# Kernel optimization log

Hardware: AMD Instinct MI355X
Metric: run time of the kernel (lower is better)

Reference implementation:

```python
import jax, jax.numpy as jnp
import numpy as np

B, N, HS = 2, 2048, 1024
H, D = 16, 64
GRID = 16           # crop_size // patch_size
SEG = 20            # d_dim = h_dim = w_dim = 2*(64//3//2)


def setup_inputs() -> dict:
    key = jax.random.key(0)
    ks = jax.random.split(key, 5)
    s = 0.02
    return {
        "hidden_states": jax.random.normal(ks[0], (B, N, HS), jnp.float32),
        "Wq": jax.random.normal(ks[1], (HS, HS), jnp.float32) * s,
        "bq": jnp.zeros((HS,), jnp.float32),
        "Wk": jax.random.normal(ks[2], (HS, HS), jnp.float32) * s,
        "bk": jnp.zeros((HS,), jnp.float32),
        "Wv": jax.random.normal(ks[3], (HS, HS), jnp.float32) * s,
        "bv": jnp.zeros((HS,), jnp.float32),
        "Wp": jax.random.normal(ks[4], (HS, HS), jnp.float32) * s,
        "bp": jnp.zeros((HS,), jnp.float32),
    }


def _rope(x, pos):
    # x: [B, H, N, d], pos: [N] int. Faithful to rotate_queries_or_keys:
    # sin/cos are TILED (concat of two copies), rotation is pairwise interleaved.
    d = x.shape[-1]
    omega = 1.0 / (10000.0 ** (jnp.arange(d // 2, dtype=x.dtype) / (d / 2.0)))
    freq = pos.astype(x.dtype)[:, None] * omega          # [N, d/2]
    sin = jnp.tile(jnp.sin(freq), (1, 2))                # [N, d]
    cos = jnp.tile(jnp.cos(freq), (1, 2))
    xp = x.reshape(x.shape[:-1] + (d // 2, 2))
    rot = jnp.stack([-xp[..., 1], xp[..., 0]], axis=-1).reshape(x.shape)
    return x * cos + rot * sin


def _apply_rope3d(qk, fpos, hpos, wpos):
    parts, s = [], 0
    for pos in (fpos, hpos, wpos):
        parts.append(_rope(qk[..., s:s + SEG], pos))
        s += SEG
    parts.append(qk[..., s:])  # pass-through remainder (4 dims)
    return jnp.concatenate(parts, axis=-1)


def reference(hidden_states, Wq, bq, Wk, bk, Wv, bv, Wp, bp):
    b, n, _ = hidden_states.shape

    def heads(x):  # [B,N,HS] -> [B,H,N,D]
        return x.reshape(b, n, H, D).transpose(0, 2, 1, 3)

    q = heads(hidden_states @ Wq.T + bq)
    k = heads(hidden_states @ Wk.T + bk)
    v = heads(hidden_states @ Wv.T + bv)

    ids = jnp.arange(n)
    tpf = GRID * GRID
    fpos = ids // tpf
    rem = ids - fpos * tpf
    hpos = rem // GRID
    wpos = rem - hpos * GRID

    q = _apply_rope3d(q, fpos, hpos, wpos)
    k = _apply_rope3d(k, fpos, hpos, wpos)

    scores = jnp.einsum('bhqd,bhkd->bhqk', q, k) * (D ** -0.5)
    probs = jax.nn.softmax(scores.astype(jnp.float32), axis=-1).astype(q.dtype)
    ctx = jnp.einsum('bhqk,bhkd->bqhd', probs, v).reshape(b, n, HS)
    return ctx @ Wp.T + bp
```

## Files before the change

kernel.cpp:

```cpp
#include <hip/hip_runtime.h>
#include <hip/hip_bf16.h>
#include <math.h>

#define BB    2
#define NN    2048
#define HSZ   1024
#define NH    16
#define HD    64
#define SEGW  20

#define LOG2E  1.4426950408889634f
#define QSCALE (0.125f * LOG2E)
#define DTHR   8.0f

typedef unsigned short u16;
typedef unsigned int   u32;
using bf16x8 = __attribute__((ext_vector_type(8))) short;
using f32x4  = __attribute__((ext_vector_type(4))) float;
using f32x16 = __attribute__((ext_vector_type(16))) float;

__device__ __forceinline__ u16 f2b(float f) {
    union { float f; u32 u; } x; x.f = f;
    u32 r = x.u + 0x7FFF + ((x.u >> 16) & 1);
    return (u16)(r >> 16);
}
__device__ __forceinline__ u16 f2bc(float f) {
    __hip_bfloat16 h = __float2bfloat16(f);
    return *reinterpret_cast<u16*>(&h);
}

__device__ __forceinline__ void gload16(void* lds, const void* g) {
    __builtin_amdgcn_global_load_lds(
        (const __attribute__((address_space(1))) void*)g,
        (__attribute__((address_space(3))) void*)lds, 16, 0, 0);
}

__device__ __forceinline__ void pswap(u32& a, u32& b) {
    asm volatile("v_permlane32_swap_b32 %0, %1" : "+v"(a), "+v"(b));
}

__global__ __launch_bounds__(256)
void cast_k(const float* __restrict__ hs, const float* __restrict__ Wq,
            const float* __restrict__ Wk, const float* __restrict__ Wv,
            const float* __restrict__ Wp, u16* __restrict__ hsb,
            u16* __restrict__ wqb, u16* __restrict__ wkb,
            u16* __restrict__ wvb, u16* __restrict__ wpb) {
    size_t idx = ((size_t)blockIdx.x * 256 + threadIdx.x) * 4;
    const float* s; u16* d; size_t o;
    const size_t HSN = 4194304, WN = 1048576;
    if      (idx < HSN)          { s = hs; d = hsb; o = idx; }
    else if (idx < HSN + WN)     { s = Wq; d = wqb; o = idx - HSN; }
    else if (idx < HSN + 2*WN)   { s = Wk; d = wkb; o = idx - HSN - WN; }
    else if (idx < HSN + 3*WN)   { s = Wv; d = wvb; o = idx - HSN - 2*WN; }
    else                         { s = Wp; d = wpb; o = idx - HSN - 3*WN; }
    float4 v = *(const float4*)(s + o);
    u32 lo = f2b(v.x) | ((u32)f2b(v.y) << 16);
    u32 hi = f2b(v.z) | ((u32)f2b(v.w) << 16);
    *(uint2*)(d + o) = uint2{lo, hi};
}

__global__ void rope_table_k(float* __restrict__ tab) {
    int n = blockIdx.x, d = threadIdx.x;
    float c = 1.f, s = 0.f;
    if (d < 3 * SEGW) {
        int seg = d / SEGW;
        int jj  = (d % SEGW) % (SEGW / 2);
        int rem = n & 255;
        int pos = (seg == 0) ? (n >> 8) : ((seg == 1) ? (rem >> 4) : (rem & 15));
        float omega = powf(10000.f, -(float)jj / 10.f);
        float fr = (float)pos * omega;
        s = sinf(fr); c = cosf(fr);
    }
    tab[(n * 64 + d) * 2 + 0] = c;
    tab[(n * 64 + d) * 2 + 1] = s;
}

__device__ __forceinline__
void gemm_body(const u16* __restrict__ X, const u16* __restrict__ Wb,
               const float* __restrict__ bias, void* __restrict__ out,
               const float* __restrict__ tab, int mode) {
    __shared__ u16 As[2][128 * 32];
    __shared__ u16 Bs[2][128 * 32];

    const int t  = threadIdx.x;
    const int w  = t >> 6;
    const int l  = t & 63;
    const int flat = blockIdx.x + (blockIdx.y << 3);
    const int o0 = (flat >> 5) * 128;
    const int m0 = (flat & 31) * 128;
    const int wr = (w >> 1) * 64;
    const int wc = (w & 1) * 64;

    const int ch  = (w << 6) + l;
    const int rA0 = ch >> 2,         cA0 = (((ch & 3) ^ (rA0 & 3))) * 8;
    const int rA1 = (ch + 256) >> 2, cA1 = (((ch & 3) ^ (rA1 & 3))) * 8;
    const int kbyte = (((l >> 4) ^ (l & 3)) << 4);

    f32x4 acc[4][4] = {};

    gload16(As[0] + ((w << 6)) * 8,       X  + (size_t)(m0 + rA0) * HSZ + cA0);
    gload16(As[0] + (256 + (w << 6)) * 8, X  + (size_t)(m0 + rA1) * HSZ + cA1);
    gload16(Bs[0] + ((w << 6)) * 8,       Wb + (size_t)(o0 + rA0) * HSZ + cA0);
    gload16(Bs[0] + (256 + (w << 6)) * 8, Wb + (size_t)(o0 + rA1) * HSZ + cA1);
    __syncthreads();

    int cur = 0;
    for (int k0 = 0; k0 < HSZ; k0 += 32, cur ^= 1) {
        if (k0 + 32 < HSZ) {
            int kn = k0 + 32;
            gload16(As[cur ^ 1] + ((w << 6)) * 8,       X  + (size_t)(m0 + rA0) * HSZ + kn + cA0);
            gload16(As[cur ^ 1] + (256 + (w << 6)) * 8, X  + (size_t)(m0 + rA1) * HSZ + kn + cA1);
            gload16(Bs[cur ^ 1] + ((w << 6)) * 8,       Wb + (size_t)(o0 + rA0) * HSZ + kn + cA0);
            gload16(Bs[cur ^ 1] + (256 + (w << 6)) * 8, Wb + (size_t)(o0 + rA1) * HSZ + kn + cA1);
        }
        bf16x8 af[4], bfr[4];
#pragma unroll
        for (int i = 0; i < 4; ++i) {
            int row = wr + i * 16 + (l & 15);
            af[i] = *(const bf16x8*)((const char*)As[cur] + row * 64 + kbyte);
        }
#pragma unroll
        for (int j = 0; j < 4; ++j) {
            int row = wc + j * 16 + (l & 15);
            bfr[j] = *(const bf16x8*)((const char*)Bs[cur] + row * 64 + kbyte);
        }
        __builtin_amdgcn_s_setprio(1);
#pragma unroll
        for (int i = 0; i < 4; ++i)
#pragma unroll
            for (int j = 0; j < 4; ++j)
                acc[i][j] = __builtin_amdgcn_mfma_f32_16x16x32_bf16(af[i], bfr[j], acc[i][j], 0, 0, 0);
        __builtin_amdgcn_s_setprio(0);
        __syncthreads();
    }

#pragma unroll
    for (int j = 0; j < 4; ++j) {
        int oc = o0 + wc + j * 16 + (l & 15);
        int h  = oc >> 6;
        int d  = oc & 63;
        float bv = bias[oc];
        if (mode == 2) {
#pragma unroll
            for (int rt = 0; rt < 4; ++rt) {
                int base = m0 + wr + rt * 16 + (l >> 4) * 4;
                int b_ = base >> 11, n0 = base & (NN - 1);
                u16 e[4];
#pragma unroll
                for (int r = 0; r < 4; ++r) e[r] = f2b(acc[rt][j][r] + bv);
                u32 lo = e[0] | ((u32)e[1] << 16);
                u32 hi = e[2] | ((u32)e[3] << 16);
                u16* vp = (u16*)out + (((size_t)b_ * NH + h) * HD + d) * NN + n0;
                *(uint2*)vp = uint2{lo, hi};
            }
        } else if (mode == 3) {
#pragma unroll
            for (int rt = 0; rt < 4; ++rt)
#pragma unroll
                for (int r = 0; r < 4; ++r) {
                    int m = m0 + wr + rt * 16 + (l >> 4) * 4 + r;
                    ((float*)out)[(size_t)m * HSZ + oc] = acc[rt][j][r] + bv;
                }
        } else {
            float scl = (mode == 0) ? QSCALE : 1.f;
#pragma unroll
            for (int rt = 0; rt < 4; ++rt)
#pragma unroll
                for (int r = 0; r < 4; ++r) {
                    int m = m0 + wr + rt * 16 + (l >> 4) * 4 + r;
                    int n = m & (NN - 1), b_ = m >> 11;
                    float v = acc[rt][j][r] + bv;
                    float2 cs = ((const float2*)tab)[n * 64 + d];
                    float part = __shfl_xor(v, 1);
                    float vr = (l & 1) ? fmaf(part, cs.y, v * cs.x)
                                       : fmaf(-part, cs.y, v * cs.x);
                    u16* qp = (u16*)out + (((size_t)b_ * NH + h) * NN + n) * HD + d;
                    *qp = f2b(vr * scl);
                }
        }
    }
}

__global__ __launch_bounds__(256)
void qkv_k(const u16* __restrict__ X,
           const u16* __restrict__ Wq, const u16* __restrict__ Wk, const u16* __restrict__ Wv,
           const float* __restrict__ bq, const float* __restrict__ bk, const float* __restrict__ bv,
           u16* __restrict__ qo, u16* __restrict__ ko, u16* __restrict__ vo,
           const float* __restrict__ tab) {
    int z = blockIdx.z;
    const u16* W   = (z == 0) ? Wq : (z == 1) ? Wk : Wv;
    const float* b = (z == 0) ? bq : (z == 1) ? bk : bv;
    u16* o         = (z == 0) ? qo : (z == 1) ? ko : vo;
    gemm_body(X, W, b, o, tab, z);
}

__global__ __launch_bounds__(256)
void projo_k(const u16* __restrict__ X, const u16* __restrict__ W,
             const float* __restrict__ b, float* __restrict__ out) {
    gemm_body(X, W, b, out, nullptr, 3);
}

__global__ __launch_bounds__(256)
void attn_mfma_k(const u16* __restrict__ Qb, const u16* __restrict__ Kb,
                 const u16* __restrict__ Vtb, u16* __restrict__ ctxb) {
    __shared__ u16 KVs[2][2][64 * 64];

    const int t = threadIdx.x, w = t >> 6, l = t & 63;
    const int h = l >> 5;
    int f  = blockIdx.y * 16 + blockIdx.x;
    int bh = (f & 7) * 4 + ((f >> 3) & 3);
    int qt = f >> 5;
    const int b_ = bh >> 4, hd = bh & 15;

    const u16* Qg = Qb + ((size_t)bh * NN + qt * 128) * HD;
    const u16* Kg = Kb + (size_t)bh * NN * HD;
    const u16* Vg = Vtb + (size_t)bh * HD * NN;

    const int xr   = (l & 7) << 4;
    const int h16  = h * 16;
    const int rowo = (l & 31) * 128;
    int kb4[4];
#pragma unroll
    for (int ks = 0; ks < 4; ++ks) kb4[ks] = ((ks * 32) | h16) ^ xr;

    const int ch  = w * 64 + l;
    const int r0  = ch >> 3,          sl0 = (ch & 7) ^ (r0 & 7);
    const int r1  = (ch + 256) >> 3,  sl1 = (ch & 7) ^ (r1 & 7);

#pragma unroll
    for (int s = 0; s < 4; ++s) {
        int c = s * 256 + ch;
        int row = c >> 3, sl = (c & 7) ^ (row & 7);
        gload16(&KVs[0][0][0] + (s * 256 + w * 64) * 8, Qg + row * HD + sl * 8);
    }
    __syncthreads();
    bf16x8 qf[4];
    {
        const char* Ql = (const char*)&KVs[0][0][0];
        int qrow = (w * 32 + (l & 31)) * 128;
#pragma unroll
        for (int ks = 0; ks < 4; ++ks)
            qf[ks] = *(const bf16x8*)(Ql + qrow + kb4[ks]);
    }
    __syncthreads();

    gload16(&KVs[0][0][0] + (w * 64) * 8,        Kg + (size_t)r0 * HD + sl0 * 8);
    gload16(&KVs[0][0][0] + (256 + w * 64) * 8,  Kg + (size_t)r1 * HD + sl1 * 8);
    gload16(&KVs[0][1][0] + (w * 64) * 8,        Vg + (size_t)r0 * NN + sl0 * 8);
    gload16(&KVs[0][1][0] + (256 + w * 64) * 8,  Vg + (size_t)r1 * NN + sl1 * 8);
    __syncthreads();

    float m_i = -INFINITY, l_i = 0.f;
    f32x16 oa0 = {}, oa1 = {};

    int cur = 0;
    for (int kt = 0; kt < NN / 64; ++kt, cur ^= 1) {
        if (kt + 1 < NN / 64) {
            int nx = (kt + 1) * 64;
            gload16(&KVs[cur ^ 1][0][0] + (w * 64) * 8,       Kg + (size_t)(nx + r0) * HD + sl0 * 8);
            gload16(&KVs[cur ^ 1][0][0] + (256 + w * 64) * 8, Kg + (size_t)(nx + r1) * HD + sl1 * 8);
            gload16(&KVs[cur ^ 1][1][0] + (w * 64) * 8,       Vg + (size_t)r0 * NN + nx + sl0 * 8);
            gload16(&KVs[cur ^ 1][1][0] + (256 + w * 64) * 8, Vg + (size_t)r1 * NN + nx + sl1 * 8);
        }

        const char* Kl = (const char*)&KVs[cur][0][0];
        f32x16 sa0 = {}, sa1 = {};
        __builtin_amdgcn_s_setprio(1);
#pragma unroll
        for (int ks = 0; ks < 4; ++ks) {
            bf16x8 k0 = *(const bf16x8*)(Kl + rowo + kb4[ks]);
            bf16x8 k1 = *(const bf16x8*)(Kl + 4096 + rowo + kb4[ks]);
            sa0 = __builtin_amdgcn_mfma_f32_32x32x16_bf16(k0, qf[ks], sa0, 0, 0, 0);
            sa1 = __builtin_amdgcn_mfma_f32_32x32x16_bf16(k1, qf[ks], sa1, 0, 0, 0);
        }
        __builtin_amdgcn_s_setprio(0);

        float mx8[8];
#pragma unroll
        for (int j = 0; j < 8; ++j)
            mx8[j] = fmaxf(fmaxf(sa0[j], sa0[j + 8]), fmaxf(sa1[j], sa1[j + 8]));
        float pm = fmaxf(fmaxf(fmaxf(mx8[0], mx8[1]), fmaxf(mx8[2], mx8[3])),
                         fmaxf(fmaxf(mx8[4], mx8[5]), fmaxf(mx8[6], mx8[7])));
        if (__any(pm > m_i + DTHR)) {
            float mx = fmaxf(pm, __shfl_xor(pm, 32));
            float mn = fmaxf(m_i, mx);
            float alpha = __builtin_amdgcn_exp2f(m_i - mn);
            m_i = mn;
            l_i *= alpha;
#pragma unroll
            for (int r = 0; r < 16; ++r) { oa0[r] *= alpha; oa1[r] *= alpha; }
        }

        u32 o_[16];
        float ls0 = 0.f, ls1 = 0.f, ls2 = 0.f, ls3 = 0.f;
#pragma unroll
        for (int j = 0; j < 8; ++j) {
            float pa = __builtin_amdgcn_exp2f(sa0[2 * j]     - m_i);
            float pb = __builtin_amdgcn_exp2f(sa0[2 * j + 1] - m_i);
            float pc = __builtin_amdgcn_exp2f(sa1[2 * j]     - m_i);
            float pd = __builtin_amdgcn_exp2f(sa1[2 * j + 1] - m_i);
            ls0 += pa; ls1 += pb; ls2 += pc; ls3 += pd;
            o_[j]     = (u32)f2bc(pa) | ((u32)f2bc(pb) << 16);
            o_[8 + j] = (u32)f2bc(pc) | ((u32)f2bc(pd) << 16);
        }
        l_i += (ls0 + ls1) + (ls2 + ls3);

        pswap(o_[0], o_[2]);   pswap(o_[1], o_[3]);
        pswap(o_[4], o_[6]);   pswap(o_[5], o_[7]);
        pswap(o_[8], o_[10]);  pswap(o_[9], o_[11]);
        pswap(o_[12], o_[14]); pswap(o_[13], o_[15]);

        const char* Vl = (const char*)&KVs[cur][1][0];
        __builtin_amdgcn_s_setprio(1);
#pragma unroll
        for (int ks2 = 0; ks2 < 4; ++ks2) {
            union { u32 u[4]; bf16x8 v; } fr;
            fr.u[0] = o_[4 * ks2 + 0]; fr.u[1] = o_[4 * ks2 + 1];
            fr.u[2] = o_[4 * ks2 + 2]; fr.u[3] = o_[4 * ks2 + 3];
            bf16x8 v0 = *(const bf16x8*)(Vl + rowo + kb4[ks2]);
            bf16x8 v1 = *(const bf16x8*)(Vl + 4096 + rowo + kb4[ks2]);
            oa0 = __builtin_amdgcn_mfma_f32_32x32x16_bf16(v0, fr.v, oa0, 0, 0, 0);
            oa1 = __builtin_amdgcn_mfma_f32_32x32x16_bf16(v1, fr.v, oa1, 0, 0, 0);
        }
        __builtin_amdgcn_s_setprio(0);

        __syncthreads();
    }

    float lt = l_i + __shfl_xor(l_i, 32);
    float inv = 1.f / lt;
    int n = qt * 128 + w * 32 + (l & 31);
    u16* op = ctxb + ((size_t)b_ * NN + n) * HSZ + hd * 64;
#pragma unroll
    for (int dt = 0; dt < 2; ++dt) {
        const f32x16& oa = dt ? oa1 : oa0;
#pragma unroll
        for (int rg = 0; rg < 4; ++rg) {
            int d0 = 4 * h + 8 * rg + 32 * dt;
            u16 e0 = f2bc(oa[4 * rg + 0] * inv);
            u16 e1 = f2bc(oa[4 * rg + 1] * inv);
            u16 e2 = f2bc(oa[4 * rg + 2] * inv);
            u16 e3 = f2bc(oa[4 * rg + 3] * inv);
            *(uint2*)(op + d0) = uint2{e0 | ((u32)e1 << 16), e2 | ((u32)e3 << 16)};
        }
    }
}

extern "C" void kernel_launch(void* const* d_in, const int* in_sizes, int n_in,
                              void* d_out, int out_size, void* d_ws, size_t ws_size,
                              hipStream_t stream) {
    (void)in_sizes; (void)n_in; (void)out_size; (void)ws_size;
    const float* hs = (const float*)d_in[0];
    const float* Wq = (const float*)d_in[1];
    const float* bq = (const float*)d_in[2];
    const float* Wk = (const float*)d_in[3];
    const float* bk = (const float*)d_in[4];
    const float* Wv = (const float*)d_in[5];
    const float* bv = (const float*)d_in[6];
    const float* Wp = (const float*)d_in[7];
    const float* bp = (const float*)d_in[8];

    char* ws = (char*)d_ws;
    u16*   hsb  = (u16*)(ws);
    u16*   Wqb  = (u16*)(ws + 8388608);
    u16*   Wkb  = (u16*)(ws + 10485760);
    u16*   Wvb  = (u16*)(ws + 12582912);
    u16*   Wpb  = (u16*)(ws + 14680064);
    u16*   qb   = (u16*)(ws + 16777216);
    u16*   kb   = (u16*)(ws + 25165824);
    u16*   vtb  = (u16*)(ws + 33554432);
    u16*   ctxb = (u16*)(ws + 41943040);
    float* tab  = (float*)(ws + 50331648);

    cast_k<<<8192, 256, 0, stream>>>(hs, Wq, Wk, Wv, Wp, hsb, Wqb, Wkb, Wvb, Wpb);
    rope_table_k<<<NN, 64, 0, stream>>>(tab);

    qkv_k<<<dim3(HSZ / 128, (BB * NN) / 128, 3), 256, 0, stream>>>(
        hsb, Wqb, Wkb, Wvb, bq, bk, bv, qb, kb, vtb, tab);

    attn_mfma_k<<<dim3(NN / 128, BB * NH), 256, 0, stream>>>(qb, kb, vtb, ctxb);

    projo_k<<<dim3(HSZ / 128, (BB * NN) / 128), 256, 0, stream>>>(ctxb, Wpb, bp, (float*)d_out);
}
```

Before: 140.4 us.

## Split attention KV across warp pairs and load GEMM B fragments directly from global

The attention kernel now gives each warp two 32-query subtiles and half of each 64-key tile, so one K fragment load feeds two MFMAs. Each warp pair keeps its own running max and sum, and the partial outputs are merged through shared memory at the end. The projection GEMM drops the shared-memory staging of the weight tile and loads B fragments straight from global into registers, prefetched one step ahead. This trades LDS traffic for uncoalesced global loads and more registers, plus an extra cross-warp merge with its barrier.

```diff
diff --git a/kernel.cpp b/kernel.cpp
--- a/kernel.cpp
+++ b/kernel.cpp
@@ -80,7 +80,6 @@
                const float* __restrict__ bias, void* __restrict__ out,
                const float* __restrict__ tab, int mode) {
     __shared__ u16 As[2][128 * 32];
-    __shared__ u16 Bs[2][128 * 32];
 
     const int t  = threadIdx.x;
     const int w  = t >> 6;
@@ -96,41 +95,46 @@
     const int rA1 = (ch + 256) >> 2, cA1 = (((ch & 3) ^ (rA1 & 3))) * 8;
     const int kbyte = (((l >> 4) ^ (l & 3)) << 4);
 
+    const u16* bp[4];
+#pragma unroll
+    for (int j = 0; j < 4; ++j)
+        bp[j] = Wb + (size_t)(o0 + wc + j * 16 + (l & 15)) * HSZ + ((l >> 4) << 3);
+
     f32x4 acc[4][4] = {};
-
-    gload16(As[0] + ((w << 6)) * 8,       X  + (size_t)(m0 + rA0) * HSZ + cA0);
-    gload16(As[0] + (256 + (w << 6)) * 8, X  + (size_t)(m0 + rA1) * HSZ + cA1);
-    gload16(Bs[0] + ((w << 6)) * 8,       Wb + (size_t)(o0 + rA0) * HSZ + cA0);
-    gload16(Bs[0] + (256 + (w << 6)) * 8, Wb + (size_t)(o0 + rA1) * HSZ + cA1);
+    bf16x8 bc[4], bn[4];
+
+    gload16(As[0] + ((w << 6)) * 8,       X + (size_t)(m0 + rA0) * HSZ + cA0);
+    gload16(As[0] + (256 + (w << 6)) * 8, X + (size_t)(m0 + rA1) * HSZ + cA1);
+#pragma unroll
+    for (int j = 0; j < 4; ++j) bc[j] = *(const bf16x8*)(bp[j]);
     __syncthreads();
 
     int cur = 0;
     for (int k0 = 0; k0 < HSZ; k0 += 32, cur ^= 1) {
         if (k0 + 32 < HSZ) {
             int kn = k0 + 32;
-            gload16(As[cur ^ 1] + ((w << 6)) * 8,       X  + (size_t)(m0 + rA0) * HSZ + kn + cA0);
-            gload16(As[cur ^ 1] + (256 + (w << 6)) * 8, X  + (size_t)(m0 + rA1) * HSZ + kn + cA1);
-            gload16(Bs[cur ^ 1] + ((w << 6)) * 8,       Wb + (size_t)(o0 + rA0) * HSZ + kn + cA0);
-            gload16(Bs[cur ^ 1] + (256 + (w << 6)) * 8, Wb + (size_t)(o0 + rA1) * HSZ + kn + cA1);
-        }
-        bf16x8 af[4], bfr[4];
+            gload16(As[cur ^ 1] + ((w << 6)) * 8,       X + (size_t)(m0 + rA0) * HSZ + kn + cA0);
+            gload16(As[cur ^ 1] + (256 + (w << 6)) * 8, X + (size_t)(m0 + rA1) * HSZ + kn + cA1);
+#pragma unroll
+            for (int j = 0; j < 4; ++j) bn[j] = *(const bf16x8*)(bp[j] + kn);
+        }
+        bf16x8 af[4];
 #pragma unroll
         for (int i = 0; i < 4; ++i) {
             int row = wr + i * 16 + (l & 15);
             af[i] = *(const bf16x8*)((const char*)As[cur] + row * 64 + kbyte);
         }
-#pragma unroll
-        for (int j = 0; j < 4; ++j) {
-            int row = wc + j * 16 + (l & 15);
-            bfr[j] = *(const bf16x8*)((const char*)Bs[cur] + row * 64 + kbyte);
-        }
         __builtin_amdgcn_s_setprio(1);
 #pragma unroll
         for (int i = 0; i < 4; ++i)
 #pragma unroll
             for (int j = 0; j < 4; ++j)
-                acc[i][j] = __builtin_amdgcn_mfma_f32_16x16x32_bf16(af[i], bfr[j], acc[i][j], 0, 0, 0);
+                acc[i][j] = __builtin_amdgcn_mfma_f32_16x16x32_bf16(af[i], bc[j], acc[i][j], 0, 0, 0);
         __builtin_amdgcn_s_setprio(0);
+        if (k0 + 32 < HSZ) {
+#pragma unroll
+            for (int j = 0; j < 4; ++j) bc[j] = bn[j];
+        }
         __syncthreads();
     }
 
@@ -204,9 +208,12 @@
 void attn_mfma_k(const u16* __restrict__ Qb, const u16* __restrict__ Kb,
                  const u16* __restrict__ Vtb, u16* __restrict__ ctxb) {
     __shared__ u16 KVs[2][2][64 * 64];
+    __shared__ float2 MLs[2][2][32];
 
     const int t = threadIdx.x, w = t >> 6, l = t & 63;
     const int h = l >> 5;
+    const int qh = w & 1, kh = w >> 1;
+    const int q = l & 31;
     int f  = blockIdx.y * 16 + blockIdx.x;
     int bh = (f & 7) * 4 + ((f >> 3) & 3);
     int qt = f >> 5;
@@ -216,16 +223,15 @@
     const u16* Kg = Kb + (size_t)bh * NN * HD;
     const u16* Vg = Vtb + (size_t)bh * HD * NN;
 
-    const int xr   = (l & 7) << 4;
-    const int h16  = h * 16;
-    const int rowo = (l & 31) * 128;
+    const int xr  = (l & 7) << 4;
+    const int h16 = h * 16;
     int kb4[4];
 #pragma unroll
     for (int ks = 0; ks < 4; ++ks) kb4[ks] = ((ks * 32) | h16) ^ xr;
 
     const int ch  = w * 64 + l;
-    const int r0  = ch >> 3,          sl0 = (ch & 7) ^ (r0 & 7);
-    const int r1  = (ch + 256) >> 3,  sl1 = (ch & 7) ^ (r1 & 7);
+    const int r0  = ch >> 3,         sl0 = (ch & 7) ^ (r0 & 7);
+    const int r1  = (ch + 256) >> 3, sl1 = (ch & 7) ^ (r1 & 7);
 
 #pragma unroll
     for (int s = 0; s < 4; ++s) {
@@ -234,25 +240,28 @@
         gload16(&KVs[0][0][0] + (s * 256 + w * 64) * 8, Qg + row * HD + sl * 8);
     }
     __syncthreads();
-    bf16x8 qf[4];
+    bf16x8 qf[2][4];
     {
         const char* Ql = (const char*)&KVs[0][0][0];
-        int qrow = (w * 32 + (l & 31)) * 128;
-#pragma unroll
-        for (int ks = 0; ks < 4; ++ks)
-            qf[ks] = *(const bf16x8*)(Ql + qrow + kb4[ks]);
+#pragma unroll
+        for (int qs = 0; qs < 2; ++qs)
+#pragma unroll
+            for (int ks = 0; ks < 4; ++ks)
+                qf[qs][ks] = *(const bf16x8*)(Ql + (qh * 64 + qs * 32 + q) * 128 + kb4[ks]);
     }
     __syncthreads();
 
-    gload16(&KVs[0][0][0] + (w * 64) * 8,        Kg + (size_t)r0 * HD + sl0 * 8);
-    gload16(&KVs[0][0][0] + (256 + w * 64) * 8,  Kg + (size_t)r1 * HD + sl1 * 8);
-    gload16(&KVs[0][1][0] + (w * 64) * 8,        Vg + (size_t)r0 * NN + sl0 * 8);
-    gload16(&KVs[0][1][0] + (256 + w * 64) * 8,  Vg + (size_t)r1 * NN + sl1 * 8);
+    gload16(&KVs[0][0][0] + (w * 64) * 8,       Kg + (size_t)r0 * HD + sl0 * 8);
+    gload16(&KVs[0][0][0] + (256 + w * 64) * 8, Kg + (size_t)r1 * HD + sl1 * 8);
+    gload16(&KVs[0][1][0] + (w * 64) * 8,       Vg + (size_t)r0 * NN + sl0 * 8);
+    gload16(&KVs[0][1][0] + (256 + w * 64) * 8, Vg + (size_t)r1 * NN + sl1 * 8);
     __syncthreads();
 
-    float m_i = -INFINITY, l_i = 0.f;
-    f32x16 oa0 = {}, oa1 = {};
-
+    float m_i[2] = {-INFINITY, -INFINITY};
+    float l_i[2] = {0.f, 0.f};
+    f32x16 oa[2][2] = {};
+
+    const int rowk = (kh * 32 + q) * 128;
     int cur = 0;
     for (int kt = 0; kt < NN / 64; ++kt, cur ^= 1) {
         if (kt + 1 < NN / 64) {
@@ -264,84 +273,124 @@
         }
 
         const char* Kl = (const char*)&KVs[cur][0][0];
-        f32x16 sa0 = {}, sa1 = {};
+        f32x16 sa[2] = {};
         __builtin_amdgcn_s_setprio(1);
 #pragma unroll
         for (int ks = 0; ks < 4; ++ks) {
-            bf16x8 k0 = *(const bf16x8*)(Kl + rowo + kb4[ks]);
-            bf16x8 k1 = *(const bf16x8*)(Kl + 4096 + rowo + kb4[ks]);
-            sa0 = __builtin_amdgcn_mfma_f32_32x32x16_bf16(k0, qf[ks], sa0, 0, 0, 0);
-            sa1 = __builtin_amdgcn_mfma_f32_32x32x16_bf16(k1, qf[ks], sa1, 0, 0, 0);
+            bf16x8 kf = *(const bf16x8*)(Kl + rowk + kb4[ks]);
+            sa[0] = __builtin_amdgcn_mfma_f32_32x32x16_bf16(kf, qf[0][ks], sa[0], 0, 0, 0);
+            sa[1] = __builtin_amdgcn_mfma_f32_32x32x16_bf16(kf, qf[1][ks], sa[1], 0, 0, 0);
         }
         __builtin_amdgcn_s_setprio(0);
 
-        float mx8[8];
-#pragma unroll
-        for (int j = 0; j < 8; ++j)
-            mx8[j] = fmaxf(fmaxf(sa0[j], sa0[j + 8]), fmaxf(sa1[j], sa1[j + 8]));
-        float pm = fmaxf(fmaxf(fmaxf(mx8[0], mx8[1]), fmaxf(mx8[2], mx8[3])),
-                         fmaxf(fmaxf(mx8[4], mx8[5]), fmaxf(mx8[6], mx8[7])));
-        if (__any(pm > m_i + DTHR)) {
-            float mx = fmaxf(pm, __shfl_xor(pm, 32));
-            float mn = fmaxf(m_i, mx);
-            float alpha = __builtin_amdgcn_exp2f(m_i - mn);
-            m_i = mn;
-            l_i *= alpha;
-#pragma unroll
-            for (int r = 0; r < 16; ++r) { oa0[r] *= alpha; oa1[r] *= alpha; }
-        }
-
-        u32 o_[16];
-        float ls0 = 0.f, ls1 = 0.f, ls2 = 0.f, ls3 = 0.f;
-#pragma unroll
-        for (int j = 0; j < 8; ++j) {
-            float pa = __builtin_amdgcn_exp2f(sa0[2 * j]     - m_i);
-            float pb = __builtin_amdgcn_exp2f(sa0[2 * j + 1] - m_i);
-            float pc = __builtin_amdgcn_exp2f(sa1[2 * j]     - m_i);
-            float pd = __builtin_amdgcn_exp2f(sa1[2 * j + 1] - m_i);
-            ls0 += pa; ls1 += pb; ls2 += pc; ls3 += pd;
-            o_[j]     = (u32)f2bc(pa) | ((u32)f2bc(pb) << 16);
-            o_[8 + j] = (u32)f2bc(pc) | ((u32)f2bc(pd) << 16);
-        }
-        l_i += (ls0 + ls1) + (ls2 + ls3);
-
-        pswap(o_[0], o_[2]);   pswap(o_[1], o_[3]);
-        pswap(o_[4], o_[6]);   pswap(o_[5], o_[7]);
-        pswap(o_[8], o_[10]);  pswap(o_[9], o_[11]);
-        pswap(o_[12], o_[14]); pswap(o_[13], o_[15]);
+        float pm[2];
+#pragma unroll
+        for (int qs = 0; qs < 2; ++qs) {
+            float t8[8];
+#pragma unroll
+            for (int j = 0; j < 8; ++j) t8[j] = fmaxf(sa[qs][2 * j], sa[qs][2 * j + 1]);
+            float a0 = fmaxf(t8[0], t8[1]), a1 = fmaxf(t8[2], t8[3]);
+            float a2 = fmaxf(t8[4], t8[5]), a3 = fmaxf(t8[6], t8[7]);
+            pm[qs] = fmaxf(fmaxf(a0, a1), fmaxf(a2, a3));
+        }
+        if (__any((pm[0] > m_i[0] + DTHR) | (pm[1] > m_i[1] + DTHR))) {
+#pragma unroll
+            for (int qs = 0; qs < 2; ++qs) {
+                float mx = fmaxf(pm[qs], __shfl_xor(pm[qs], 32));
+                float mn = fmaxf(m_i[qs], mx);
+                float alpha = __builtin_amdgcn_exp2f(m_i[qs] - mn);
+                m_i[qs] = mn;
+                l_i[qs] *= alpha;
+#pragma unroll
+                for (int r = 0; r < 16; ++r) { oa[qs][0][r] *= alpha; oa[qs][1][r] *= alpha; }
+            }
+        }
+
+        u32 oq[2][8];
+#pragma unroll
+        for (int qs = 0; qs < 2; ++qs) {
+            float ls = 0.f;
+#pragma unroll
+            for (int j = 0; j < 8; ++j) {
+                float pa = __builtin_amdgcn_exp2f(sa[qs][2 * j]     - m_i[qs]);
+                float pb = __builtin_amdgcn_exp2f(sa[qs][2 * j + 1] - m_i[qs]);
+                ls += pa + pb;
+                oq[qs][j] = (u32)f2bc(pa) | ((u32)f2bc(pb) << 16);
+            }
+            l_i[qs] += ls;
+            pswap(oq[qs][0], oq[qs][2]); pswap(oq[qs][1], oq[qs][3]);
+            pswap(oq[qs][4], oq[qs][6]); pswap(oq[qs][5], oq[qs][7]);
+        }
 
         const char* Vl = (const char*)&KVs[cur][1][0];
         __builtin_amdgcn_s_setprio(1);
 #pragma unroll
-        for (int ks2 = 0; ks2 < 4; ++ks2) {
-            union { u32 u[4]; bf16x8 v; } fr;
-            fr.u[0] = o_[4 * ks2 + 0]; fr.u[1] = o_[4 * ks2 + 1];
-            fr.u[2] = o_[4 * ks2 + 2]; fr.u[3] = o_[4 * ks2 + 3];
-            bf16x8 v0 = *(const bf16x8*)(Vl + rowo + kb4[ks2]);
-            bf16x8 v1 = *(const bf16x8*)(Vl + 4096 + rowo + kb4[ks2]);
-            oa0 = __builtin_amdgcn_mfma_f32_32x32x16_bf16(v0, fr.v, oa0, 0, 0, 0);
-            oa1 = __builtin_amdgcn_mfma_f32_32x32x16_bf16(v1, fr.v, oa1, 0, 0, 0);
+        for (int ks2 = 0; ks2 < 2; ++ks2) {
+            int vb = (((kh * 2 + ks2) * 32) | h16) ^ xr;
+            bf16x8 v0 = *(const bf16x8*)(Vl + q * 128 + vb);
+            bf16x8 v1 = *(const bf16x8*)(Vl + (32 + q) * 128 + vb);
+            union { u32 u[4]; bf16x8 v; } f0, f1;
+#pragma unroll
+            for (int p = 0; p < 4; ++p) {
+                f0.u[p] = oq[0][4 * ks2 + p];
+                f1.u[p] = oq[1][4 * ks2 + p];
+            }
+            oa[0][0] = __builtin_amdgcn_mfma_f32_32x32x16_bf16(v0, f0.v, oa[0][0], 0, 0, 0);
+            oa[0][1] = __builtin_amdgcn_mfma_f32_32x32x16_bf16(v1, f0.v, oa[0][1], 0, 0, 0);
+            oa[1][0] = __builtin_amdgcn_mfma_f32_32x32x16_bf16(v0, f1.v, oa[1][0], 0, 0, 0);
+            oa[1][1] = __builtin_amdgcn_mfma_f32_32x32x16_bf16(v1, f1.v, oa[1][1], 0, 0, 0);
         }
         __builtin_amdgcn_s_setprio(0);
 
         __syncthreads();
     }
 
-    float lt = l_i + __shfl_xor(l_i, 32);
-    float inv = 1.f / lt;
-    int n = qt * 128 + w * 32 + (l & 31);
-    u16* op = ctxb + ((size_t)b_ * NN + n) * HSZ + hd * 64;
-#pragma unroll
-    for (int dt = 0; dt < 2; ++dt) {
-        const f32x16& oa = dt ? oa1 : oa0;
-#pragma unroll
-        for (int rg = 0; rg < 4; ++rg) {
-            int d0 = 4 * h + 8 * rg + 32 * dt;
-            u16 e0 = f2bc(oa[4 * rg + 0] * inv);
-            u16 e1 = f2bc(oa[4 * rg + 1] * inv);
-            u16 e2 = f2bc(oa[4 * rg + 2] * inv);
-            u16 e3 = f2bc(oa[4 * rg + 3] * inv);
-            *(uint2*)(op + d0) = uint2{e0 | ((u32)e1 << 16), e2 | ((u32)e3 << 16)};
+    float lh[2];
+#pragma unroll
+    for (int qs = 0; qs < 2; ++qs) lh[qs] = l_i[qs] + __shfl_xor(l_i[qs], 32);
+
+    float* Olds = (float*)&KVs[0][0][0];
+    if (kh == 1) {
+#pragma unroll
+        for (int qs = 0; qs < 2; ++qs) {
+            int base = ((qh * 2 + qs) * 32 + q) * 256;
+#pragma unroll
+            for (int dh = 0; dh < 2; ++dh)
+#pragma unroll
+                for (int g = 0; g < 4; ++g) {
+                    int off = (128 * dh + 32 * g + 16 * h) ^ ((q & 7) << 4);
+                    float4 v4 = {oa[qs][dh][4 * g + 0], oa[qs][dh][4 * g + 1],
+                                 oa[qs][dh][4 * g + 2], oa[qs][dh][4 * g + 3]};
+                    *(float4*)((char*)Olds + base + off) = v4;
+                }
+            if (h == 0) MLs[qh][qs][q] = float2{m_i[qs], lh[qs]};
+        }
+    }
+    __syncthreads();
+    if (kh == 0) {
+#pragma unroll
+        for (int qs = 0; qs < 2; ++qs) {
+            float2 ml1 = MLs[qh][qs][q];
+            float mM = fmaxf(m_i[qs], ml1.x);
+            float w0 = __builtin_amdgcn_exp2f(m_i[qs] - mM);
+            float w1 = __builtin_amdgcn_exp2f(ml1.x - mM);
+            float inv = 1.f / (w0 * lh[qs] + w1 * ml1.y);
+            int n = qt * 128 + qh * 64 + qs * 32 + q;
+            u16* op = ctxb + ((size_t)b_ * NN + n) * HSZ + hd * 64;
+            int base = ((qh * 2 + qs) * 32 + q) * 256;
+#pragma unroll
+            for (int dh = 0; dh < 2; ++dh)
+#pragma unroll
+                for (int g = 0; g < 4; ++g) {
+                    int off = (128 * dh + 32 * g + 16 * h) ^ ((q & 7) << 4);
+                    float4 o1 = *(const float4*)((const char*)Olds + base + off);
+                    int d0 = 8 * g + 4 * h + 32 * dh;
+                    u16 e0 = f2bc((oa[qs][dh][4 * g + 0] * w0 + o1.x * w1) * inv);
+                    u16 e1 = f2bc((oa[qs][dh][4 * g + 1] * w0 + o1.y * w1) * inv);
+                    u16 e2 = f2bc((oa[qs][dh][4 * g + 2] * w0 + o1.z * w1) * inv);
+                    u16 e3 = f2bc((oa[qs][dh][4 * g + 3] * w0 + o1.w * w1) * inv);
+                    *(uint2*)(op + d0) = uint2{e0 | ((u32)e1 << 16), e2 | ((u32)e3 << 16)};
+                }
         }
     }
 }
```

After: 188.4 us. +34.2%, slower.

## Shrink QKV/output GEMM tiles to 128x64 and drop LDS swizzle

Applied to the files above, without the earlier changes.

The shared GEMM body now computes 128x64 output tiles instead of 128x128, so each of the four waves holds a 64x32 accumulator block. This doubles the grid for the QKV and output-projection launches (16x32 blocks). The change also removes the XOR swizzle on LDS loads and reads, and drops the s_setprio hints. The intent is more blocks and higher occupancy with fewer registers per block. The cost is less data reuse per block, more global traffic for the activation tiles, and likely LDS bank conflicts from the unswizzled 64-byte row stride.

```diff
diff --git a/kernel.cpp b/kernel.cpp
--- a/kernel.cpp
+++ b/kernel.cpp
@@ -80,28 +80,27 @@
                const float* __restrict__ bias, void* __restrict__ out,
                const float* __restrict__ tab, int mode) {
     __shared__ u16 As[2][128 * 32];
-    __shared__ u16 Bs[2][128 * 32];
+    __shared__ u16 Bs[2][64 * 32];
 
     const int t  = threadIdx.x;
     const int w  = t >> 6;
     const int l  = t & 63;
-    const int flat = blockIdx.x + (blockIdx.y << 3);
-    const int o0 = (flat >> 5) * 128;
+    const int flat = blockIdx.x + (blockIdx.y << 4);
+    const int o0 = (flat >> 5) * 64;
     const int m0 = (flat & 31) * 128;
     const int wr = (w >> 1) * 64;
-    const int wc = (w & 1) * 64;
-
-    const int ch  = (w << 6) + l;
-    const int rA0 = ch >> 2,         cA0 = (((ch & 3) ^ (rA0 & 3))) * 8;
-    const int rA1 = (ch + 256) >> 2, cA1 = (((ch & 3) ^ (rA1 & 3))) * 8;
-    const int kbyte = (((l >> 4) ^ (l & 3)) << 4);
-
-    f32x4 acc[4][4] = {};
+    const int wc = (w & 1) * 32;
+
+    const int chA0 = (w << 6) + l;
+    const int rA0 = chA0 >> 2,         cA0 = (chA0 & 3) * 8;
+    const int rA1 = (chA0 + 256) >> 2, cA1 = (chA0 & 3) * 8;
+    const int rB  = chA0 >> 2,         cB  = (chA0 & 3) * 8;
+
+    f32x4 acc[4][2] = {};
 
     gload16(As[0] + ((w << 6)) * 8,       X  + (size_t)(m0 + rA0) * HSZ + cA0);
     gload16(As[0] + (256 + (w << 6)) * 8, X  + (size_t)(m0 + rA1) * HSZ + cA1);
-    gload16(Bs[0] + ((w << 6)) * 8,       Wb + (size_t)(o0 + rA0) * HSZ + cA0);
-    gload16(Bs[0] + (256 + (w << 6)) * 8, Wb + (size_t)(o0 + rA1) * HSZ + cA1);
+    gload16(Bs[0] + ((w << 6)) * 8,       Wb + (size_t)(o0 + rB) * HSZ + cB);
     __syncthreads();
 
     int cur = 0;
@@ -110,34 +109,27 @@
             int kn = k0 + 32;
             gload16(As[cur ^ 1] + ((w << 6)) * 8,       X  + (size_t)(m0 + rA0) * HSZ + kn + cA0);
             gload16(As[cur ^ 1] + (256 + (w << 6)) * 8, X  + (size_t)(m0 + rA1) * HSZ + kn + cA1);
-            gload16(Bs[cur ^ 1] + ((w << 6)) * 8,       Wb + (size_t)(o0 + rA0) * HSZ + kn + cA0);
-            gload16(Bs[cur ^ 1] + (256 + (w << 6)) * 8, Wb + (size_t)(o0 + rA1) * HSZ + kn + cA1);
-        }
-        bf16x8 af[4], bfr[4];
-#pragma unroll
-        for (int i = 0; i < 4; ++i) {
-            int row = wr + i * 16 + (l & 15);
-            af[i] = *(const bf16x8*)((const char*)As[cur] + row * 64 + kbyte);
-        }
-#pragma unroll
-        for (int j = 0; j < 4; ++j) {
-            int row = wc + j * 16 + (l & 15);
-            bfr[j] = *(const bf16x8*)((const char*)Bs[cur] + row * 64 + kbyte);
-        }
-        __builtin_amdgcn_s_setprio(1);
+            gload16(Bs[cur ^ 1] + ((w << 6)) * 8,       Wb + (size_t)(o0 + rB) * HSZ + kn + cB);
+        }
+        bf16x8 af[4], bfr[2];
 #pragma unroll
         for (int i = 0; i < 4; ++i)
-#pragma unroll
-            for (int j = 0; j < 4; ++j)
+            af[i] = *(const bf16x8*)(As[cur] + (wr + i * 16 + (l & 15)) * 32 + (l >> 4) * 8);
+#pragma unroll
+        for (int j = 0; j < 2; ++j)
+            bfr[j] = *(const bf16x8*)(Bs[cur] + (wc + j * 16 + (l & 15)) * 32 + (l >> 4) * 8);
+#pragma unroll
+        for (int i = 0; i < 4; ++i)
+#pragma unroll
+            for (int j = 0; j < 2; ++j)
                 acc[i][j] = __builtin_amdgcn_mfma_f32_16x16x32_bf16(af[i], bfr[j], acc[i][j], 0, 0, 0);
-        __builtin_amdgcn_s_setprio(0);
         __syncthreads();
     }
 
-#pragma unroll
-    for (int j = 0; j < 4; ++j) {
-        int oc = o0 + wc + j * 16 + (l & 15);
-        int h  = oc >> 6;
+    const int h = o0 >> 6;
+#pragma unroll
+    for (int ct = 0; ct < 2; ++ct) {
+        int oc = o0 + wc + ct * 16 + (l & 15);
         int d  = oc & 63;
         float bv = bias[oc];
         if (mode == 2) {
@@ -147,7 +139,7 @@
                 int b_ = base >> 11, n0 = base & (NN - 1);
                 u16 e[4];
 #pragma unroll
-                for (int r = 0; r < 4; ++r) e[r] = f2b(acc[rt][j][r] + bv);
+                for (int r = 0; r < 4; ++r) e[r] = f2b(acc[rt][ct][r] + bv);
                 u32 lo = e[0] | ((u32)e[1] << 16);
                 u32 hi = e[2] | ((u32)e[3] << 16);
                 u16* vp = (u16*)out + (((size_t)b_ * NH + h) * HD + d) * NN + n0;
@@ -159,7 +151,7 @@
 #pragma unroll
                 for (int r = 0; r < 4; ++r) {
                     int m = m0 + wr + rt * 16 + (l >> 4) * 4 + r;
-                    ((float*)out)[(size_t)m * HSZ + oc] = acc[rt][j][r] + bv;
+                    ((float*)out)[(size_t)m * HSZ + oc] = acc[rt][ct][r] + bv;
                 }
         } else {
             float scl = (mode == 0) ? QSCALE : 1.f;
@@ -169,7 +161,7 @@
                 for (int r = 0; r < 4; ++r) {
                     int m = m0 + wr + rt * 16 + (l >> 4) * 4 + r;
                     int n = m & (NN - 1), b_ = m >> 11;
-                    float v = acc[rt][j][r] + bv;
+                    float v = acc[rt][ct][r] + bv;
                     float2 cs = ((const float2*)tab)[n * 64 + d];
                     float part = __shfl_xor(v, 1);
                     float vr = (l & 1) ? fmaf(part, cs.y, v * cs.x)
@@ -375,10 +367,10 @@
     cast_k<<<8192, 256, 0, stream>>>(hs, Wq, Wk, Wv, Wp, hsb, Wqb, Wkb, Wvb, Wpb);
     rope_table_k<<<NN, 64, 0, stream>>>(tab);
 
-    qkv_k<<<dim3(HSZ / 128, (BB * NN) / 128, 3), 256, 0, stream>>>(
+    qkv_k<<<dim3(16, 32, 3), 256, 0, stream>>>(
         hsb, Wqb, Wkb, Wvb, bq, bk, bv, qb, kb, vtb, tab);
 
     attn_mfma_k<<<dim3(NN / 128, BB * NH), 256, 0, stream>>>(qb, kb, vtb, ctxb);
 
-    projo_k<<<dim3(HSZ / 128, (BB * NN) / 128), 256, 0, stream>>>(ctxb, Wpb, bp, (float*)d_out);
-}
+    projo_k<<<dim3(16, 32), 256, 0, stream>>>(ctxb, Wpb, bp, (float*)d_out);
+}
```

Result: slower. 145.7 us (+3.7%).

## Split attention over key range with combine pass; stream GEMM weights from registers

Applied to the files above, without the earlier changes.

Attention now runs as two key-range splits per query tile, which doubles the grid. Each split writes unnormalised fp32 partial outputs plus its running max and sum, and a new combine kernel merges them into bf16 context. The intent is better CU occupancy, since the old grid of 512 blocks was small for the device. The GEMM body also drops the shared-memory B tile and loads weight fragments straight from global memory into registers with one-step prefetch. This trades more global traffic and an extra kernel pass for fewer LDS accesses. Wp is now cast in a separate kernel after attention because its buffer reuses workspace space that the partials overwrite.

```diff
diff --git a/kernel.cpp b/kernel.cpp
--- a/kernel.cpp
+++ b/kernel.cpp
@@ -42,21 +42,28 @@
 __global__ __launch_bounds__(256)
 void cast_k(const float* __restrict__ hs, const float* __restrict__ Wq,
             const float* __restrict__ Wk, const float* __restrict__ Wv,
-            const float* __restrict__ Wp, u16* __restrict__ hsb,
-            u16* __restrict__ wqb, u16* __restrict__ wkb,
-            u16* __restrict__ wvb, u16* __restrict__ wpb) {
+            u16* __restrict__ hsb, u16* __restrict__ wqb,
+            u16* __restrict__ wkb, u16* __restrict__ wvb) {
     size_t idx = ((size_t)blockIdx.x * 256 + threadIdx.x) * 4;
     const float* s; u16* d; size_t o;
     const size_t HSN = 4194304, WN = 1048576;
     if      (idx < HSN)          { s = hs; d = hsb; o = idx; }
     else if (idx < HSN + WN)     { s = Wq; d = wqb; o = idx - HSN; }
     else if (idx < HSN + 2*WN)   { s = Wk; d = wkb; o = idx - HSN - WN; }
-    else if (idx < HSN + 3*WN)   { s = Wv; d = wvb; o = idx - HSN - 2*WN; }
-    else                         { s = Wp; d = wpb; o = idx - HSN - 3*WN; }
+    else                         { s = Wv; d = wvb; o = idx - HSN - 2*WN; }
     float4 v = *(const float4*)(s + o);
     u32 lo = f2b(v.x) | ((u32)f2b(v.y) << 16);
     u32 hi = f2b(v.z) | ((u32)f2b(v.w) << 16);
     *(uint2*)(d + o) = uint2{lo, hi};
+}
+
+__global__ __launch_bounds__(256)
+void castwp_k(const float* __restrict__ Wp, u16* __restrict__ wpb) {
+    size_t idx = ((size_t)blockIdx.x * 256 + threadIdx.x) * 4;
+    float4 v = *(const float4*)(Wp + idx);
+    u32 lo = f2b(v.x) | ((u32)f2b(v.y) << 16);
+    u32 hi = f2b(v.z) | ((u32)f2b(v.w) << 16);
+    *(uint2*)(wpb + idx) = uint2{lo, hi};
 }
 
 __global__ void rope_table_k(float* __restrict__ tab) {
@@ -80,7 +87,6 @@
                const float* __restrict__ bias, void* __restrict__ out,
                const float* __restrict__ tab, int mode) {
     __shared__ u16 As[2][128 * 32];
-    __shared__ u16 Bs[2][128 * 32];
 
     const int t  = threadIdx.x;
     const int w  = t >> 6;
@@ -96,41 +102,46 @@
     const int rA1 = (ch + 256) >> 2, cA1 = (((ch & 3) ^ (rA1 & 3))) * 8;
     const int kbyte = (((l >> 4) ^ (l & 3)) << 4);
 
+    const u16* bp[4];
+#pragma unroll
+    for (int j = 0; j < 4; ++j)
+        bp[j] = Wb + (size_t)(o0 + wc + j * 16 + (l & 15)) * HSZ + ((l >> 4) << 3);
+
     f32x4 acc[4][4] = {};
-
-    gload16(As[0] + ((w << 6)) * 8,       X  + (size_t)(m0 + rA0) * HSZ + cA0);
-    gload16(As[0] + (256 + (w << 6)) * 8, X  + (size_t)(m0 + rA1) * HSZ + cA1);
-    gload16(Bs[0] + ((w << 6)) * 8,       Wb + (size_t)(o0 + rA0) * HSZ + cA0);
-    gload16(Bs[0] + (256 + (w << 6)) * 8, Wb + (size_t)(o0 + rA1) * HSZ + cA1);
+    bf16x8 bc[4], bn[4];
+
+    gload16(As[0] + ((w << 6)) * 8,       X + (size_t)(m0 + rA0) * HSZ + cA0);
+    gload16(As[0] + (256 + (w << 6)) * 8, X + (size_t)(m0 + rA1) * HSZ + cA1);
+#pragma unroll
+    for (int j = 0; j < 4; ++j) bc[j] = *(const bf16x8*)(bp[j]);
     __syncthreads();
 
     int cur = 0;
     for (int k0 = 0; k0 < HSZ; k0 += 32, cur ^= 1) {
         if (k0 + 32 < HSZ) {
             int kn = k0 + 32;
-            gload16(As[cur ^ 1] + ((w << 6)) * 8,       X  + (size_t)(m0 + rA0) * HSZ + kn + cA0);
-            gload16(As[cur ^ 1] + (256 + (w << 6)) * 8, X  + (size_t)(m0 + rA1) * HSZ + kn + cA1);
-            gload16(Bs[cur ^ 1] + ((w << 6)) * 8,       Wb + (size_t)(o0 + rA0) * HSZ + kn + cA0);
-            gload16(Bs[cur ^ 1] + (256 + (w << 6)) * 8, Wb + (size_t)(o0 + rA1) * HSZ + kn + cA1);
-        }
-        bf16x8 af[4], bfr[4];
+            gload16(As[cur ^ 1] + ((w << 6)) * 8,       X + (size_t)(m0 + rA0) * HSZ + kn + cA0);
+            gload16(As[cur ^ 1] + (256 + (w << 6)) * 8, X + (size_t)(m0 + rA1) * HSZ + kn + cA1);
+#pragma unroll
+            for (int j = 0; j < 4; ++j) bn[j] = *(const bf16x8*)(bp[j] + kn);
+        }
+        bf16x8 af[4];
 #pragma unroll
         for (int i = 0; i < 4; ++i) {
             int row = wr + i * 16 + (l & 15);
             af[i] = *(const bf16x8*)((const char*)As[cur] + row * 64 + kbyte);
         }
-#pragma unroll
-        for (int j = 0; j < 4; ++j) {
-            int row = wc + j * 16 + (l & 15);
-            bfr[j] = *(const bf16x8*)((const char*)Bs[cur] + row * 64 + kbyte);
-        }
         __builtin_amdgcn_s_setprio(1);
 #pragma unroll
         for (int i = 0; i < 4; ++i)
 #pragma unroll
             for (int j = 0; j < 4; ++j)
-                acc[i][j] = __builtin_amdgcn_mfma_f32_16x16x32_bf16(af[i], bfr[j], acc[i][j], 0, 0, 0);
+                acc[i][j] = __builtin_amdgcn_mfma_f32_16x16x32_bf16(af[i], bc[j], acc[i][j], 0, 0, 0);
         __builtin_amdgcn_s_setprio(0);
+        if (k0 + 32 < HSZ) {
+#pragma unroll
+            for (int j = 0; j < 4; ++j) bc[j] = bn[j];
+        }
         __syncthreads();
     }
 
@@ -202,7 +213,9 @@
 
 __global__ __launch_bounds__(256)
 void attn_mfma_k(const u16* __restrict__ Qb, const u16* __restrict__ Kb,
-                 const u16* __restrict__ Vtb, u16* __restrict__ ctxb) {
+                 const u16* __restrict__ Vtb, float* __restrict__ po0,
+                 float* __restrict__ po1, float* __restrict__ pm,
+                 float* __restrict__ pl) {
     __shared__ u16 KVs[2][2][64 * 64];
 
     const int t = threadIdx.x, w = t >> 6, l = t & 63;
@@ -210,7 +223,9 @@
     int f  = blockIdx.y * 16 + blockIdx.x;
     int bh = (f & 7) * 4 + ((f >> 3) & 3);
     int qt = f >> 5;
-    const int b_ = bh >> 4, hd = bh & 15;
+    const int sp = blockIdx.z;
+    float* po = sp ? po1 : po0;
+    const int kt0 = sp * 16;
 
     const u16* Qg = Qb + ((size_t)bh * NN + qt * 128) * HD;
     const u16* Kg = Kb + (size_t)bh * NN * HD;
@@ -244,18 +259,18 @@
     }
     __syncthreads();
 
-    gload16(&KVs[0][0][0] + (w * 64) * 8,        Kg + (size_t)r0 * HD + sl0 * 8);
-    gload16(&KVs[0][0][0] + (256 + w * 64) * 8,  Kg + (size_t)r1 * HD + sl1 * 8);
-    gload16(&KVs[0][1][0] + (w * 64) * 8,        Vg + (size_t)r0 * NN + sl0 * 8);
-    gload16(&KVs[0][1][0] + (256 + w * 64) * 8,  Vg + (size_t)r1 * NN + sl1 * 8);
+    gload16(&KVs[0][0][0] + (w * 64) * 8,        Kg + (size_t)(kt0 * 64 + r0) * HD + sl0 * 8);
+    gload16(&KVs[0][0][0] + (256 + w * 64) * 8,  Kg + (size_t)(kt0 * 64 + r1) * HD + sl1 * 8);
+    gload16(&KVs[0][1][0] + (w * 64) * 8,        Vg + (size_t)r0 * NN + kt0 * 64 + sl0 * 8);
+    gload16(&KVs[0][1][0] + (256 + w * 64) * 8,  Vg + (size_t)r1 * NN + kt0 * 64 + sl1 * 8);
     __syncthreads();
 
     float m_i = -INFINITY, l_i = 0.f;
     f32x16 oa0 = {}, oa1 = {};
 
     int cur = 0;
-    for (int kt = 0; kt < NN / 64; ++kt, cur ^= 1) {
-        if (kt + 1 < NN / 64) {
+    for (int kt = kt0; kt < kt0 + 16; ++kt, cur ^= 1) {
+        if (kt + 1 < kt0 + 16) {
             int nx = (kt + 1) * 64;
             gload16(&KVs[cur ^ 1][0][0] + (w * 64) * 8,       Kg + (size_t)(nx + r0) * HD + sl0 * 8);
             gload16(&KVs[cur ^ 1][0][0] + (256 + w * 64) * 8, Kg + (size_t)(nx + r1) * HD + sl1 * 8);
@@ -279,10 +294,10 @@
 #pragma unroll
         for (int j = 0; j < 8; ++j)
             mx8[j] = fmaxf(fmaxf(sa0[j], sa0[j + 8]), fmaxf(sa1[j], sa1[j + 8]));
-        float pm = fmaxf(fmaxf(fmaxf(mx8[0], mx8[1]), fmaxf(mx8[2], mx8[3])),
-                         fmaxf(fmaxf(mx8[4], mx8[5]), fmaxf(mx8[6], mx8[7])));
-        if (__any(pm > m_i + DTHR)) {
-            float mx = fmaxf(pm, __shfl_xor(pm, 32));
+        float pmv = fmaxf(fmaxf(fmaxf(mx8[0], mx8[1]), fmaxf(mx8[2], mx8[3])),
+                          fmaxf(fmaxf(mx8[4], mx8[5]), fmaxf(mx8[6], mx8[7])));
+        if (__any(pmv > m_i + DTHR)) {
+            float mx = fmaxf(pmv, __shfl_xor(pmv, 32));
             float mn = fmaxf(m_i, mx);
             float alpha = __builtin_amdgcn_exp2f(m_i - mn);
             m_i = mn;
@@ -327,22 +342,53 @@
         __syncthreads();
     }
 
-    float lt = l_i + __shfl_xor(l_i, 32);
-    float inv = 1.f / lt;
-    int n = qt * 128 + w * 32 + (l & 31);
-    u16* op = ctxb + ((size_t)b_ * NN + n) * HSZ + hd * 64;
+    float lh = l_i + __shfl_xor(l_i, 32);
+    int q = l & 31;
+    int n = qt * 128 + w * 32 + q;
+    float* pop = po + ((size_t)bh * NN + n) * HD;
 #pragma unroll
     for (int dt = 0; dt < 2; ++dt) {
         const f32x16& oa = dt ? oa1 : oa0;
 #pragma unroll
         for (int rg = 0; rg < 4; ++rg) {
             int d0 = 4 * h + 8 * rg + 32 * dt;
-            u16 e0 = f2bc(oa[4 * rg + 0] * inv);
-            u16 e1 = f2bc(oa[4 * rg + 1] * inv);
-            u16 e2 = f2bc(oa[4 * rg + 2] * inv);
-            u16 e3 = f2bc(oa[4 * rg + 3] * inv);
-            *(uint2*)(op + d0) = uint2{e0 | ((u32)e1 << 16), e2 | ((u32)e3 << 16)};
-        }
+            float4 v4 = {oa[4 * rg + 0], oa[4 * rg + 1], oa[4 * rg + 2], oa[4 * rg + 3]};
+            *(float4*)(pop + d0) = v4;
+        }
+    }
+    if (h == 0) {
+        pm[sp * 65536 + bh * NN + n] = m_i;
+        pl[sp * 65536 + bh * NN + n] = lh;
+    }
+}
+
+__global__ __launch_bounds__(256)
+void combine_k(const float* __restrict__ po0, const float* __restrict__ po1,
+               const float* __restrict__ pm, const float* __restrict__ pl,
+               u16* __restrict__ ctxb) {
+    int idx = blockIdx.x * 256 + threadIdx.x;
+    int row = idx >> 2;
+    int dp  = (idx & 3) * 16;
+    int bh = row >> 11, n = row & 2047;
+    int b_ = bh >> 4, h = bh & 15;
+    float m0 = pm[row], m1 = pm[65536 + row];
+    float l0 = pl[row], l1 = pl[65536 + row];
+    float m = fmaxf(m0, m1);
+    float w0 = __builtin_amdgcn_exp2f(m0 - m);
+    float w1 = __builtin_amdgcn_exp2f(m1 - m);
+    float inv = 1.f / (w0 * l0 + w1 * l1);
+    const float* a = po0 + (size_t)row * 64 + dp;
+    const float* b = po1 + (size_t)row * 64 + dp;
+    u16* o = ctxb + ((size_t)b_ * NN + n) * HSZ + h * 64 + dp;
+#pragma unroll
+    for (int j = 0; j < 4; ++j) {
+        float4 x = ((const float4*)a)[j];
+        float4 y = ((const float4*)b)[j];
+        u16 e0 = f2b((x.x * w0 + y.x * w1) * inv);
+        u16 e1 = f2b((x.y * w0 + y.y * w1) * inv);
+        u16 e2 = f2b((x.z * w0 + y.z * w1) * inv);
+        u16 e3 = f2b((x.w * w0 + y.w * w1) * inv);
+        *(uint2*)(o + j * 4) = uint2{e0 | ((u32)e1 << 16), e2 | ((u32)e3 << 16)};
     }
 }
 
@@ -365,20 +411,27 @@
     u16*   Wqb  = (u16*)(ws + 8388608);
     u16*   Wkb  = (u16*)(ws + 10485760);
     u16*   Wvb  = (u16*)(ws + 12582912);
-    u16*   Wpb  = (u16*)(ws + 14680064);
     u16*   qb   = (u16*)(ws + 16777216);
     u16*   kb   = (u16*)(ws + 25165824);
     u16*   vtb  = (u16*)(ws + 33554432);
     u16*   ctxb = (u16*)(ws + 41943040);
     float* tab  = (float*)(ws + 50331648);
-
-    cast_k<<<8192, 256, 0, stream>>>(hs, Wq, Wk, Wv, Wp, hsb, Wqb, Wkb, Wvb, Wpb);
+    float* pm   = (float*)(ws + 50331648);
+    float* pl   = (float*)(ws + 50331648 + 524288);
+    float* po0  = (float*)(ws);
+    float* po1  = (float*)(ws + 51380224);
+    u16*   Wpb  = (u16*)(ws);
+
+    cast_k<<<7168, 256, 0, stream>>>(hs, Wq, Wk, Wv, hsb, Wqb, Wkb, Wvb);
     rope_table_k<<<NN, 64, 0, stream>>>(tab);
 
-    qkv_k<<<dim3(HSZ / 128, (BB * NN) / 128, 3), 256, 0, stream>>>(
+    qkv_k<<<dim3(8, 32, 3), 256, 0, stream>>>(
         hsb, Wqb, Wkb, Wvb, bq, bk, bv, qb, kb, vtb, tab);
 
-    attn_mfma_k<<<dim3(NN / 128, BB * NH), 256, 0, stream>>>(qb, kb, vtb, ctxb);
-
-    projo_k<<<dim3(HSZ / 128, (BB * NN) / 128), 256, 0, stream>>>(ctxb, Wpb, bp, (float*)d_out);
-}
+    attn_mfma_k<<<dim3(16, 32, 2), 256, 0, stream>>>(qb, kb, vtb, po0, po1, pm, pl);
+
+    combine_k<<<1024, 256, 0, stream>>>(po0, po1, pm, pl, ctxb);
+    castwp_k<<<1024, 256, 0, stream>>>(Wp, Wpb);
+
+    projo_k<<<dim3(8, 32), 256, 0, stream>>>(ctxb, Wpb, bp, (float*)d_out);
+}
```

After: 177.1 us. +26.1%, slower.
